# Kernel tuning notes

Hardware: AMD Instinct MI355X
Metric: run time of the kernel (lower is better)

The kernel has to match this reference:

```python
import jax, jax.numpy as jnp
import numpy as np

N = 50000       # nodes
F_IN = 256
F_OUT = 64
H = 4           # heads
DEG = 16        # avg degree (random edges per node)
NEG_SLOPE = 0.2


def setup_inputs() -> dict:
    key = jax.random.key(0)
    k_h, k_e, k_w, k_fc = jax.random.split(key, 4)
    h = jax.random.normal(k_h, (N, F_IN), dtype=jnp.float32)
    # random edges + explicit self-loops so every node has >= 1 out-edge
    e_rand = jax.random.randint(k_e, (2, N * DEG), 0, N, dtype=jnp.int64)
    loops = jnp.tile(jnp.arange(N, dtype=jnp.int64)[None, :], (2, 1))
    edge_index = jnp.concatenate([e_rand, loops], axis=1)  # [2, 850000]
    # Glorot-uniform-like scales
    s_w = np.sqrt(6.0 / (F_IN + F_OUT)).astype(np.float32)
    s_a = np.sqrt(6.0 / (2 * F_OUT + 1)).astype(np.float32)
    w = jax.random.uniform(k_w, (H, F_IN, F_OUT), jnp.float32, -s_w, s_w)
    fc = jax.random.uniform(k_fc, (H, 2 * F_OUT, 1), jnp.float32, -s_a, s_a)
    bias = jnp.zeros((F_OUT,), jnp.float32)
    return {"h": h, "edge_index": edge_index, "w": w, "fc": fc, "bias": bias}


def reference(h, edge_index, w, fc, bias):
    # GAT forward, vectorized over edges (dropout is identity at inference).
    n = h.shape[0]
    f_out = w.shape[2]
    src, dst = edge_index[0], edge_index[1]           # [E]
    h_prime = jnp.einsum('nf,hfo->hno', h, w)          # [H, N, F]
    a = fc[..., 0]                                     # [H, 2F]
    a_src, a_dst = a[:, :f_out], a[:, f_out:]          # [H, F] each
    s_src = jnp.einsum('hnf,hf->hn', h_prime, a_src)   # [H, N] score of center node
    s_dst = jnp.einsum('hnf,hf->hn', h_prime, a_dst)   # [H, N] score of neighbor
    e = jax.nn.leaky_relu(s_src[:, src] + s_dst[:, dst], NEG_SLOPE)  # [H, E]
    e = e.T                                            # [E, H]
    # segment softmax over edges grouped by source node
    seg_max = jax.ops.segment_max(e, src, num_segments=n)   # [N, H]
    ex = jnp.exp(e - seg_max[src])                           # [E, H]
    denom = jax.ops.segment_sum(ex, src, num_segments=n)    # [N, H]
    alpha = ex / denom[src]                                  # [E, H]
    # scatter-aggregate: out_i = sum_{j in N(i)} alpha_ij * Wh_j
    msgs = alpha[:, :, None] * jnp.transpose(h_prime[:, dst, :], (1, 0, 2))  # [E, H, F]
    out = jax.ops.segment_sum(msgs, src, num_segments=n)    # [N, H, F]
    return out.mean(axis=1) + bias                           # [N, F]
```

## Files before the change

kernel.cpp:

```cpp
#include <hip/hip_runtime.h>
#include <cfloat>

#define FIN 256
#define FOUT 64
#define NH 4
#define NEG_SLOPE 0.2f
#define SLOTS 64
#define BCAP 3072
#define P1T 4096

typedef __bf16 bf16x8 __attribute__((ext_vector_type(8)));
typedef float f32x4 __attribute__((ext_vector_type(4)));

__device__ __forceinline__ ushort f2bf(float f) {
    return (ushort)((__float_as_uint(f) + 0x8000u) >> 16);
}
__device__ __forceinline__ float bf2f(ushort u) {
    return __uint_as_float(((unsigned)u) << 16);
}
__device__ __forceinline__ float lrelu(float x) {
    return (x >= 0.f) ? x : NEG_SLOPE * x;
}

__global__ __launch_bounds__(256) void k0_wconv(const float* __restrict__ w,
                                                ushort* __restrict__ wt,
                                                int* __restrict__ gcur, int gn)
{
    if ((int)blockIdx.x < 256) {
        const int g = blockIdx.x * 256 + threadIdx.x;
        const int hh  = g >> 14;
        const int rem = g & 16383;
        const int c   = rem >> 8;
        const int k   = rem & 255;
        wt[g] = f2bf(w[(((hh << 8) | k) << 6) | c]);
    } else {
        const int g = ((int)blockIdx.x - 256) * 256 + threadIdx.x;
        if (g < gn) gcur[g] = 0;
    }
}

#define ASTRIDE 280
#define OSTRIDE 260
__global__ __launch_bounds__(256) void k1(
    const int* __restrict__ ei, int E, int nbuck,
    int* __restrict__ gcur, unsigned* __restrict__ barea, int p1B,
    const float* __restrict__ h, const ushort* __restrict__ wt,
    const float* __restrict__ fc, ushort* __restrict__ hp,
    float* __restrict__ s_src, float* __restrict__ s_dst, int N)
{
    __shared__ ushort lds[64 * ASTRIDE];
    const int tid = threadIdx.x;

    if ((int)blockIdx.x < p1B) {
        int* lcnt        = (int*)lds;
        int* lscan       = lcnt + 512;
        int* lbase       = lscan + 512;
        unsigned* ledges = (unsigned*)(lbase + 512);

        for (int b = tid; b < 512; b += 256) lcnt[b] = 0;
        __syncthreads();

        const int e0 = (int)blockIdx.x * P1T;
        const int cnt_total = min(P1T, E - e0);
        int s[16], d[16];
#pragma unroll
        for (int i = 0; i < 16; ++i) {
            const int e = e0 + i * 256 + tid;
            if (e < E) {
                s[i] = ei[e];
                d[i] = ei[E + e];
                atomicAdd(&lcnt[s[i] >> 7], 1);
            } else {
                s[i] = -1; d[i] = 0;
            }
        }
        __syncthreads();

        if (tid < 64) {
            int vals[8], sum = 0;
#pragma unroll
            for (int k = 0; k < 8; ++k) { vals[k] = lcnt[tid * 8 + k]; sum += vals[k]; }
            int x = sum;
#pragma unroll
            for (int dd = 1; dd < 64; dd <<= 1) {
                const int t = __shfl_up(x, dd);
                if (tid >= dd) x += t;
            }
            int run = x - sum;
#pragma unroll
            for (int k = 0; k < 8; ++k) { lscan[tid * 8 + k] = run; run += vals[k]; }
        }
        __syncthreads();

        for (int b = tid; b < nbuck; b += 256) {
            const int c = lcnt[b];
            lbase[b] = c ? atomicAdd(&gcur[b * 16], c) : 0;
        }
        __syncthreads();
        for (int b = tid; b < 512; b += 256) lcnt[b] = 0;
        __syncthreads();

#pragma unroll
        for (int i = 0; i < 16; ++i) {
            if (s[i] >= 0) {
                const int b = s[i] >> 7;
                const int r = atomicAdd(&lcnt[b], 1);
                ledges[lscan[b] + r] =
                    ((unsigned)b << 23) | ((unsigned)(s[i] & 127) << 16) |
                    (unsigned)d[i];
            }
        }
        __syncthreads();

        for (int j = tid; j < cnt_total; j += 256) {
            const unsigned p = ledges[j];
            const int b = (int)(p >> 23);
            const int pos = lbase[b] + (j - lscan[b]);
            if (pos < BCAP)
                barea[(size_t)b * BCAP + pos] = p & 0x007FFFFFu;
        }
        return;
    }

    const int bid = (int)blockIdx.x - p1B;
    const int n0 = bid * 64;

#pragma unroll
    for (int half = 0; half < 2; ++half) {
        float4 va[8];
#pragma unroll
        for (int i = 0; i < 8; ++i) {
            const int idx = half * 2048 + i * 256 + tid;
            const int row  = idx >> 6;
            const int quad = idx & 63;
            const int n = n0 + row;
            va[i] = (n < N) ? ((const float4*)(h + (size_t)n * FIN))[quad]
                            : make_float4(0.f, 0.f, 0.f, 0.f);
        }
#pragma unroll
        for (int i = 0; i < 8; ++i) {
            const int idx = half * 2048 + i * 256 + tid;
            const int row  = idx >> 6;
            const int quad = idx & 63;
            ushort4 bv;
            bv.x = f2bf(va[i].x); bv.y = f2bf(va[i].y);
            bv.z = f2bf(va[i].z); bv.w = f2bf(va[i].w);
            *(ushort4*)&lds[row * ASTRIDE + quad * 4] = bv;
        }
    }
    __syncthreads();

    const int head = tid >> 6;
    const int lane = tid & 63;
    const int lrow = lane & 15;
    const int lq   = lane >> 4;

    const ushort* wth = wt + head * (64 * 256);

    f32x4 acc[4][4];
#pragma unroll
    for (int mt = 0; mt < 4; ++mt)
#pragma unroll
        for (int nt = 0; nt < 4; ++nt)
            acc[mt][nt] = (f32x4){0.f, 0.f, 0.f, 0.f};

#pragma unroll
    for (int kt = 0; kt < 8; ++kt) {
        const int kof = kt * 32 + lq * 8;
        bf16x8 bfr[4];
#pragma unroll
        for (int nt = 0; nt < 4; ++nt)
            bfr[nt] = *(const bf16x8*)&wth[(nt * 16 + lrow) * 256 + kof];
        bf16x8 af[4];
#pragma unroll
        for (int mt = 0; mt < 4; ++mt)
            af[mt] = *(const bf16x8*)&lds[(mt * 16 + lrow) * ASTRIDE + kof];
#pragma unroll
        for (int nt = 0; nt < 4; ++nt)
#pragma unroll
            for (int mt = 0; mt < 4; ++mt)
                acc[mt][nt] = __builtin_amdgcn_mfma_f32_16x16x32_bf16(
                    af[mt], bfr[nt], acc[mt][nt], 0, 0, 0);
    }

    float as_[4], ad_[4];
#pragma unroll
    for (int nt = 0; nt < 4; ++nt) {
        as_[nt] = fc[head * 2 * FOUT + nt * 16 + lrow];
        ad_[nt] = fc[head * 2 * FOUT + FOUT + nt * 16 + lrow];
    }
#pragma unroll
    for (int mt = 0; mt < 4; ++mt) {
        const int rbase = n0 + mt * 16 + lq * 4;
#pragma unroll
        for (int r = 0; r < 4; ++r) {
            const int n = rbase + r;
            float ps = 0.f, pd = 0.f;
#pragma unroll
            for (int nt = 0; nt < 4; ++nt) {
                const float v = acc[mt][nt][r];
                ps = fmaf(v, as_[nt], ps);
                pd = fmaf(v, ad_[nt], pd);
            }
            ps += __shfl_xor(ps, 1); pd += __shfl_xor(pd, 1);
            ps += __shfl_xor(ps, 2); pd += __shfl_xor(pd, 2);
            ps += __shfl_xor(ps, 4); pd += __shfl_xor(pd, 4);
            ps += __shfl_xor(ps, 8); pd += __shfl_xor(pd, 8);
            if (lrow == 0 && n < N) {
                s_src[(size_t)n * NH + head] = ps;
                s_dst[(size_t)n * NH + head] = pd;
            }
        }
    }

    __syncthreads();
#pragma unroll
    for (int mt = 0; mt < 4; ++mt)
#pragma unroll
        for (int r = 0; r < 4; ++r)
#pragma unroll
            for (int nt = 0; nt < 4; ++nt)
                lds[(mt * 16 + lq * 4 + r) * OSTRIDE +
                    (nt * 16 + lrow) * 4 + head] = f2bf(acc[mt][nt][r]);
    __syncthreads();
    for (int idx = tid; idx < 64 * 64; idx += 256) {
        const int row = idx >> 6;
        const int c   = idx & 63;
        const int n = n0 + row;
        if (n < N)
            *(ushort4*)&hp[(size_t)n * 256 + c * 4] =
                *(const ushort4*)&lds[row * OSTRIDE + c * 4];
    }
}

__global__ __launch_bounds__(256) void k2(
    const int* __restrict__ gcur, const unsigned* __restrict__ barea,
    ushort* __restrict__ col, int* __restrict__ cursor)
{
    __shared__ ushort colT[128 * SLOTS];
    __shared__ int cnt[128];
    const int tid = threadIdx.x;
    const int b = blockIdx.x;
    for (int i = tid; i < 128; i += 256) cnt[i] = 0;
    __syncthreads();
    int c = gcur[b * 16];
    if (c > BCAP) c = BCAP;
    for (int j = tid; j < c; j += 256) {
        const unsigned p = barea[(size_t)b * BCAP + j];
        const int sl = (int)(p >> 16);
        const int r = atomicAdd(&cnt[sl], 1);
        if (r < SLOTS) colT[sl * SLOTS + r] = (ushort)(p & 0xFFFFu);
    }
    __syncthreads();
    const size_t gbase = (size_t)b * 128 * SLOTS;
    for (int idx = tid; idx < 128 * SLOTS / 4; idx += 256)
        *(ushort4*)&col[gbase + (size_t)idx * 4] =
            *(const ushort4*)&colT[idx * 4];
    for (int i = tid; i < 128; i += 256)
        cursor[b * 128 + i] = cnt[i];
}

__global__ __launch_bounds__(256) void k_agg(
    const int* __restrict__ cursor, const ushort* __restrict__ col,
    const ushort* __restrict__ hp,
    const float* __restrict__ s_src, const float* __restrict__ s_dst,
    const float* __restrict__ bias, float* __restrict__ out, int N, int base)
{
    const int wid  = threadIdx.x >> 6;
    const int lane = threadIdx.x & 63;
    const int n    = base + blockIdx.x * 4 + wid;
    if (n >= N) return;

    const size_t start = (size_t)n * SLOTS;
    const int deg = min(cursor[n], SLOTS);
    const float4 ssn = ((const float4*)s_src)[n];
    const float4* sd4 = (const float4*)s_dst;

    float4 acc = make_float4(0.f, 0.f, 0.f, 0.f);

    int dreg = 0;
    float4 x = make_float4(-FLT_MAX, -FLT_MAX, -FLT_MAX, -FLT_MAX);
    if (lane < deg) {
        dreg = col[start + lane];
        const float4 sd = sd4[dreg];
        x.x = lrelu(ssn.x + sd.x);
        x.y = lrelu(ssn.y + sd.y);
        x.z = lrelu(ssn.z + sd.z);
        x.w = lrelu(ssn.w + sd.w);
    }
    float4 m = x;
#pragma unroll
    for (int d = 32; d; d >>= 1) {
        m.x = fmaxf(m.x, __shfl_xor(m.x, d));
        m.y = fmaxf(m.y, __shfl_xor(m.y, d));
        m.z = fmaxf(m.z, __shfl_xor(m.z, d));
        m.w = fmaxf(m.w, __shfl_xor(m.w, d));
    }
    float4 e = make_float4(0.f, 0.f, 0.f, 0.f);
    if (lane < deg) {
        e.x = __expf(x.x - m.x);
        e.y = __expf(x.y - m.y);
        e.z = __expf(x.z - m.z);
        e.w = __expf(x.w - m.w);
    }
    float4 s = e;
#pragma unroll
    for (int d = 32; d; d >>= 1) {
        s.x += __shfl_xor(s.x, d);
        s.y += __shfl_xor(s.y, d);
        s.z += __shfl_xor(s.z, d);
        s.w += __shfl_xor(s.w, d);
    }
    float4 alpha;
    alpha.x = e.x / s.x;
    alpha.y = e.y / s.y;
    alpha.z = e.z / s.z;
    alpha.w = e.w / s.w;

    const int nblk = (deg + 3) >> 2;
    for (int b = 0; b < nblk; ++b) {
        int dd[4]; float4 av[4]; ushort4 v[4];
#pragma unroll
        for (int u = 0; u < 4; ++u) {
            const int j = b * 4 + u;
            dd[u]   = __shfl(dreg, j);
            av[u].x = __shfl(alpha.x, j);
            av[u].y = __shfl(alpha.y, j);
            av[u].z = __shfl(alpha.z, j);
            av[u].w = __shfl(alpha.w, j);
        }
#pragma unroll
        for (int u = 0; u < 4; ++u)
            v[u] = *(const ushort4*)&hp[((size_t)dd[u] * FOUT + lane) * NH];
#pragma unroll
        for (int u = 0; u < 4; ++u) {
            acc.x = fmaf(av[u].x, bf2f(v[u].x), acc.x);
            acc.y = fmaf(av[u].y, bf2f(v[u].y), acc.y);
            acc.z = fmaf(av[u].z, bf2f(v[u].z), acc.z);
            acc.w = fmaf(av[u].w, bf2f(v[u].w), acc.w);
        }
    }

    out[(size_t)n * FOUT + lane] =
        (acc.x + acc.y + acc.z + acc.w) * 0.25f + bias[lane];
}

extern "C" void kernel_launch(void* const* d_in, const int* in_sizes, int n_in,
                              void* d_out, int out_size, void* d_ws, size_t ws_size,
                              hipStream_t stream)
{
    const float* h    = (const float*)d_in[0];
    const int*   ei   = (const int*)d_in[1];
    const float* w    = (const float*)d_in[2];
    const float* fc   = (const float*)d_in[3];
    const float* bias = (const float*)d_in[4];
    float* out = (float*)d_out;

    const int N = in_sizes[0] / FIN;
    const int E = in_sizes[1] / 2;
    const int nbuck = (N + 127) >> 7;

    char* ws = (char*)d_ws;
    auto take = [&](size_t bytes) {
        char* p = ws;
        ws += (bytes + 255) & ~(size_t)255;
        return p;
    };
    ushort*   wt      = (ushort*)take((size_t)NH * FIN * FOUT * sizeof(ushort));
    ushort*   h_prime = (ushort*)take((size_t)NH * N * FOUT * sizeof(ushort));
    float*    s_src   = (float*)take((size_t)NH * N * sizeof(float));
    float*    s_dst   = (float*)take((size_t)NH * N * sizeof(float));
    int*      cursor  = (int*)take((size_t)nbuck * 128 * sizeof(int));
    ushort*   col     = (ushort*)take((size_t)nbuck * 128 * SLOTS * sizeof(ushort));
    int*      gcur    = (int*)take((size_t)nbuck * 16 * sizeof(int));
    unsigned* barea   = (unsigned*)take((size_t)nbuck * BCAP * sizeof(unsigned));

    const int gn = nbuck * 16;
    k0_wconv<<<256 + (gn + 255) / 256, 256, 0, stream>>>(w, wt, gcur, gn);

    const int p1B   = (E + P1T - 1) / P1T;
    const int gemmB = (N + 63) / 64;
    k1<<<p1B + gemmB, 256, 0, stream>>>(ei, E, nbuck, gcur, barea, p1B,
                                        h, wt, fc, h_prime, s_src, s_dst, N);

    k2<<<nbuck, 256, 0, stream>>>(gcur, barea, col, cursor);

    const int total_blocks = (N + 3) / 4;
    const int hb = total_blocks / 2;
    k_agg<<<hb, 256, 0, stream>>>(cursor, col, h_prime, s_src, s_dst,
                                  bias, out, N, 0);
    k_agg<<<total_blocks - hb, 256, 0, stream>>>(cursor, col, h_prime,
                                                 s_src, s_dst, bias, out, N, hb * 4);
}
```

Before: 138.8 us.

## Split fused bucketing/GEMM kernel and software-pipeline weight fragment loads

The combined kernel that ran edge bucketing and the projection GEMM in different blocks of one launch is split into two separate launches. Each kernel now gets its own LDS allocation and register budget, which may improve occupancy for both. In exchange, the two stages no longer overlap on the GPU and there is one extra launch. The GEMM now double-buffers the bf16 weight fragments, prefetching the next k-tile while the MFMAs for the current one run, at the cost of more registers. The bucket kernel also masks the slot index to 7 bits.

```diff
diff --git a/kernel.cpp b/kernel.cpp
--- a/kernel.cpp
+++ b/kernel.cpp
@@ -39,91 +39,90 @@
     }
 }
 
+__global__ __launch_bounds__(256) void k1a(
+    const int* __restrict__ ei, int E, int nbuck,
+    int* __restrict__ gcur, unsigned* __restrict__ barea)
+{
+    __shared__ int lcnt[512];
+    __shared__ int lscan[512];
+    __shared__ int lbase[512];
+    __shared__ unsigned ledges[P1T];
+    const int tid = threadIdx.x;
+
+    for (int b = tid; b < 512; b += 256) lcnt[b] = 0;
+    __syncthreads();
+
+    const int e0 = (int)blockIdx.x * P1T;
+    const int cnt_total = min(P1T, E - e0);
+    int s[16], d[16];
+#pragma unroll
+    for (int i = 0; i < 16; ++i) {
+        const int e = e0 + i * 256 + tid;
+        if (e < E) {
+            s[i] = ei[e];
+            d[i] = ei[E + e];
+            atomicAdd(&lcnt[s[i] >> 7], 1);
+        } else {
+            s[i] = -1; d[i] = 0;
+        }
+    }
+    __syncthreads();
+
+    if (tid < 64) {
+        int vals[8], sum = 0;
+#pragma unroll
+        for (int k = 0; k < 8; ++k) { vals[k] = lcnt[tid * 8 + k]; sum += vals[k]; }
+        int x = sum;
+#pragma unroll
+        for (int dd = 1; dd < 64; dd <<= 1) {
+            const int t = __shfl_up(x, dd);
+            if (tid >= dd) x += t;
+        }
+        int run = x - sum;
+#pragma unroll
+        for (int k = 0; k < 8; ++k) { lscan[tid * 8 + k] = run; run += vals[k]; }
+    }
+    __syncthreads();
+
+    for (int b = tid; b < nbuck; b += 256) {
+        const int c = lcnt[b];
+        lbase[b] = c ? atomicAdd(&gcur[b * 16], c) : 0;
+    }
+    __syncthreads();
+    for (int b = tid; b < 512; b += 256) lcnt[b] = 0;
+    __syncthreads();
+
+#pragma unroll
+    for (int i = 0; i < 16; ++i) {
+        if (s[i] >= 0) {
+            const int b = s[i] >> 7;
+            const int r = atomicAdd(&lcnt[b], 1);
+            ledges[lscan[b] + r] =
+                ((unsigned)b << 23) | ((unsigned)(s[i] & 127) << 16) |
+                (unsigned)d[i];
+        }
+    }
+    __syncthreads();
+
+    for (int j = tid; j < cnt_total; j += 256) {
+        const unsigned p = ledges[j];
+        const int b = (int)(p >> 23);
+        const int pos = lbase[b] + (j - lscan[b]);
+        if (pos < BCAP)
+            barea[(size_t)b * BCAP + pos] = p & 0x007FFFFFu;
+    }
+}
+
 #define ASTRIDE 280
 #define OSTRIDE 260
-__global__ __launch_bounds__(256) void k1(
-    const int* __restrict__ ei, int E, int nbuck,
-    int* __restrict__ gcur, unsigned* __restrict__ barea, int p1B,
+__global__ __launch_bounds__(256) void k_gemm(
     const float* __restrict__ h, const ushort* __restrict__ wt,
     const float* __restrict__ fc, ushort* __restrict__ hp,
     float* __restrict__ s_src, float* __restrict__ s_dst, int N)
 {
     __shared__ ushort lds[64 * ASTRIDE];
     const int tid = threadIdx.x;
-
-    if ((int)blockIdx.x < p1B) {
-        int* lcnt        = (int*)lds;
-        int* lscan       = lcnt + 512;
-        int* lbase       = lscan + 512;
-        unsigned* ledges = (unsigned*)(lbase + 512);
-
-        for (int b = tid; b < 512; b += 256) lcnt[b] = 0;
-        __syncthreads();
-
-        const int e0 = (int)blockIdx.x * P1T;
-        const int cnt_total = min(P1T, E - e0);
-        int s[16], d[16];
-#pragma unroll
-        for (int i = 0; i < 16; ++i) {
-            const int e = e0 + i * 256 + tid;
-            if (e < E) {
-                s[i] = ei[e];
-                d[i] = ei[E + e];
-                atomicAdd(&lcnt[s[i] >> 7], 1);
-            } else {
-                s[i] = -1; d[i] = 0;
-            }
-        }
-        __syncthreads();
-
-        if (tid < 64) {
-            int vals[8], sum = 0;
-#pragma unroll
-            for (int k = 0; k < 8; ++k) { vals[k] = lcnt[tid * 8 + k]; sum += vals[k]; }
-            int x = sum;
-#pragma unroll
-            for (int dd = 1; dd < 64; dd <<= 1) {
-                const int t = __shfl_up(x, dd);
-                if (tid >= dd) x += t;
-            }
-            int run = x - sum;
-#pragma unroll
-            for (int k = 0; k < 8; ++k) { lscan[tid * 8 + k] = run; run += vals[k]; }
-        }
-        __syncthreads();
-
-        for (int b = tid; b < nbuck; b += 256) {
-            const int c = lcnt[b];
-            lbase[b] = c ? atomicAdd(&gcur[b * 16], c) : 0;
-        }
-        __syncthreads();
-        for (int b = tid; b < 512; b += 256) lcnt[b] = 0;
-        __syncthreads();
-
-#pragma unroll
-        for (int i = 0; i < 16; ++i) {
-            if (s[i] >= 0) {
-                const int b = s[i] >> 7;
-                const int r = atomicAdd(&lcnt[b], 1);
-                ledges[lscan[b] + r] =
-                    ((unsigned)b << 23) | ((unsigned)(s[i] & 127) << 16) |
-                    (unsigned)d[i];
-            }
-        }
-        __syncthreads();
-
-        for (int j = tid; j < cnt_total; j += 256) {
-            const unsigned p = ledges[j];
-            const int b = (int)(p >> 23);
-            const int pos = lbase[b] + (j - lscan[b]);
-            if (pos < BCAP)
-                barea[(size_t)b * BCAP + pos] = p & 0x007FFFFFu;
-        }
-        return;
-    }
-
-    const int bid = (int)blockIdx.x - p1B;
-    const int n0 = bid * 64;
+    const int n0 = (int)blockIdx.x * 64;
 
 #pragma unroll
     for (int half = 0; half < 2; ++half) {
@@ -164,13 +163,20 @@
         for (int nt = 0; nt < 4; ++nt)
             acc[mt][nt] = (f32x4){0.f, 0.f, 0.f, 0.f};
 
+    bf16x8 bcur[4], bnxt[4];
+#pragma unroll
+    for (int nt = 0; nt < 4; ++nt)
+        bcur[nt] = *(const bf16x8*)&wth[(nt * 16 + lrow) * 256 + lq * 8];
+
 #pragma unroll
     for (int kt = 0; kt < 8; ++kt) {
         const int kof = kt * 32 + lq * 8;
-        bf16x8 bfr[4];
-#pragma unroll
-        for (int nt = 0; nt < 4; ++nt)
-            bfr[nt] = *(const bf16x8*)&wth[(nt * 16 + lrow) * 256 + kof];
+        if (kt < 7) {
+            const int kof2 = kof + 32;
+#pragma unroll
+            for (int nt = 0; nt < 4; ++nt)
+                bnxt[nt] = *(const bf16x8*)&wth[(nt * 16 + lrow) * 256 + kof2];
+        }
         bf16x8 af[4];
 #pragma unroll
         for (int mt = 0; mt < 4; ++mt)
@@ -180,7 +186,9 @@
 #pragma unroll
             for (int mt = 0; mt < 4; ++mt)
                 acc[mt][nt] = __builtin_amdgcn_mfma_f32_16x16x32_bf16(
-                    af[mt], bfr[nt], acc[mt][nt], 0, 0, 0);
+                    af[mt], bcur[nt], acc[mt][nt], 0, 0, 0);
+#pragma unroll
+        for (int nt = 0; nt < 4; ++nt) bcur[nt] = bnxt[nt];
     }
 
     float as_[4], ad_[4];
@@ -247,7 +255,7 @@
     if (c > BCAP) c = BCAP;
     for (int j = tid; j < c; j += 256) {
         const unsigned p = barea[(size_t)b * BCAP + j];
-        const int sl = (int)(p >> 16);
+        const int sl = (int)((p >> 16) & 127);
         const int r = atomicAdd(&cnt[sl], 1);
         if (r < SLOTS) colT[sl * SLOTS + r] = (ushort)(p & 0xFFFFu);
     }
@@ -378,10 +386,11 @@
     const int gn = nbuck * 16;
     k0_wconv<<<256 + (gn + 255) / 256, 256, 0, stream>>>(w, wt, gcur, gn);
 
-    const int p1B   = (E + P1T - 1) / P1T;
-    const int gemmB = (N + 63) / 64;
-    k1<<<p1B + gemmB, 256, 0, stream>>>(ei, E, nbuck, gcur, barea, p1B,
-                                        h, wt, fc, h_prime, s_src, s_dst, N);
+    const int p1B = (E + P1T - 1) / P1T;
+    k1a<<<p1B, 256, 0, stream>>>(ei, E, nbuck, gcur, barea);
+
+    k_gemm<<<(N + 63) / 64, 256, 0, stream>>>(h, wt, fc, h_prime,
+                                              s_src, s_dst, N);
 
     k2<<<nbuck, 256, 0, stream>>>(gcur, barea, col, cursor);
 
```

Result: slower. 151.0 us (+8.8%).
